# Performance work log

Measured on AMD Instinct MI355X. Metric: run time of the kernel, lower is better.

The kernel has to match this reference:

```python
import jax, jax.numpy as jnp
import numpy as np

NP, NA, D = 100000, 50000, 128


def _sage(x_src, x_dst, src, dst, Wm, bm, Wr, n_dst):
    # PyG SAGEConv: lin_l(mean_{j in N(i)} x_j) + lin_r(x_i); lin_r has no bias
    msgs = x_src[src]                                            # [E, D] gather
    summed = jax.ops.segment_sum(msgs, dst, num_segments=n_dst)  # [n_dst, D]
    cnt = jax.ops.segment_sum(jnp.ones((src.shape[0],), x_src.dtype), dst,
                              num_segments=n_dst)
    mean = summed / jnp.maximum(cnt, 1.0)[:, None]               # empty nbhd -> 0
    return mean @ Wm + bm + x_dst @ Wr


def setup_inputs() -> dict:
    key = jax.random.key(0)
    ks = jax.random.split(key, 14)
    s = 1.0 / np.sqrt(D)
    return {
        "x_paper": jax.random.normal(ks[0], (NP, D), jnp.float32),
        "x_author": jax.random.normal(ks[1], (NA, D), jnp.float32),
        "Wmsg1": jax.random.normal(ks[2], (3, D, D), jnp.float32) * s,
        "b1": jax.random.normal(ks[3], (3, D), jnp.float32) * s,
        "Wroot1": jax.random.normal(ks[4], (3, D, D), jnp.float32) * s,
        "Wmsg2": jax.random.normal(ks[5], (3, D, D), jnp.float32) * s,
        "b2": jax.random.normal(ks[6], (3, D), jnp.float32) * s,
        "Wroot2": jax.random.normal(ks[7], (3, D, D), jnp.float32) * s,
        "ei_cites_src": jax.random.randint(ks[8], (300000,), 0, NP, jnp.int64),
        "ei_cites_dst": jax.random.randint(ks[9], (300000,), 0, NP, jnp.int64),
        "ei_writes_src": jax.random.randint(ks[10], (150000,), 0, NA, jnp.int64),
        "ei_writes_dst": jax.random.randint(ks[11], (150000,), 0, NP, jnp.int64),
        "ei_wb_src": jax.random.randint(ks[12], (150000,), 0, NP, jnp.int64),
        "ei_wb_dst": jax.random.randint(ks[13], (150000,), 0, NA, jnp.int64),
    }


def reference(x_paper, x_author, Wmsg1, b1, Wroot1, Wmsg2, b2, Wroot2,
              ei_cites_src, ei_cites_dst, ei_writes_src, ei_writes_dst,
              ei_wb_src, ei_wb_dst):
    def hetero_layer(xp, xa, Wm, b, Wr):
        # HeteroConv(aggr='sum'): sum per-edge-type SAGEConv outputs per dst type
        out_p = (_sage(xp, xp, ei_cites_src, ei_cites_dst, Wm[0], b[0], Wr[0], NP)
                 + _sage(xa, xp, ei_writes_src, ei_writes_dst, Wm[1], b[1], Wr[1], NP))
        out_a = _sage(xp, xa, ei_wb_src, ei_wb_dst, Wm[2], b[2], Wr[2], NA)
        return out_p, out_a

    hp, ha = hetero_layer(x_paper, x_author, Wmsg1, b1, Wroot1)
    hp, ha = jax.nn.relu(hp), jax.nn.relu(ha)
    op, oa = hetero_layer(hp, ha, Wmsg2, b2, Wroot2)
    return op, oa
```

## Files before the change

### kernel.cpp

```cpp
#include <hip/hip_runtime.h>

typedef unsigned short u16;
typedef unsigned int u32;
typedef __bf16 bf16x8 __attribute__((ext_vector_type(8)));
typedef float f32x4 __attribute__((ext_vector_type(4)));

#define NPAPER 100000
#define NAUTH  50000
#define NROWS_ALL (2 * NPAPER + NAUTH)

struct alignas(16) U4 { u32 a, b, c, d; };
struct alignas(8)  U2 { u32 a, b; };
struct alignas(16) F4 { float x, y, z, w; };

__device__ __forceinline__ float bf2f(u16 u) {
    union { u32 i; float f; } v; v.i = ((u32)u) << 16; return v.f;
}
__device__ __forceinline__ u16 f2bf(float f) {
    union { float f; u32 i; } v; v.f = f;
    u32 u = v.i;
    return (u16)((u + 0x7FFFu + ((u >> 16) & 1u)) >> 16);
}

__device__ __forceinline__ float ldf(const void* p, size_t i, int f32) {
    return f32 ? ((const float*)p)[i] : bf2f(((const u16*)p)[i]);
}

__global__ void detect_dtypes(const int* __restrict__ e, const u32* __restrict__ x,
                              const u32* __restrict__ w, const u32* __restrict__ bb,
                              int* __restrict__ flags)
{
    int t = threadIdx.x, wave = t >> 6, lane = t & 63;
    if (wave == 0) {
        int v = e[lane];
        unsigned long long m = __ballot((lane & 1) && v == 0);
        if (lane == 0) flags[0] = (__popcll(m) >= 24) ? 1 : 0;
    } else {
        const u32* p = (wave == 1) ? x : ((wave == 2) ? w : bb);
        u32 wd = p[lane];
        int ex = (int)((wd >> 7) & 0xFFu);
        unsigned long long m = __ballot(ex >= 105 && ex <= 140);
        if (lane == 0) flags[wave] = (__popcll(m) >= 40) ? 0 : 1;
    }
}

__global__ __launch_bounds__(256) void convert_x(
    const void* __restrict__ xp, const void* __restrict__ xa,
    u16* __restrict__ xpb, u16* __restrict__ xab, const int* __restrict__ flags)
{
    int f32 = flags[1];
    size_t i = ((size_t)blockIdx.x * 256 + threadIdx.x) * 8;
    const size_t np = (size_t)NPAPER * 128, ntot = np + (size_t)NAUTH * 128;
    if (i >= ntot) return;
    const void* s; u16* d; size_t off;
    if (i < np) { s = xp; d = xpb; off = i; }
    else        { s = xa; d = xab; off = i - np; }
    alignas(16) u16 o[8];
    if (f32) {
        const F4* f = (const F4*)((const float*)s + off);
        F4 f0 = f[0], f1 = f[1];
        o[0] = f2bf(f0.x); o[1] = f2bf(f0.y); o[2] = f2bf(f0.z); o[3] = f2bf(f0.w);
        o[4] = f2bf(f1.x); o[5] = f2bf(f1.y); o[6] = f2bf(f1.z); o[7] = f2bf(f1.w);
    } else {
        *(U4*)o = *(const U4*)((const u16*)s + off);
    }
    *(U4*)(d + off) = *(const U4*)o;
}

__device__ __forceinline__ int permcol(int j) {
    int s = j >> 6, u = j & 63, c = u >> 4, fr = u & 15;
    return s * 64 + fr * 4 + c;
}

__global__ __launch_bounds__(256) void prep_weights2(
    const void* __restrict__ Wm1, const void* __restrict__ b1, const void* __restrict__ Wr1,
    const void* __restrict__ Wm2, const void* __restrict__ b2, const void* __restrict__ Wr2,
    u16* __restrict__ WTp1, u16* __restrict__ WTa1,
    float* __restrict__ biasp1, float* __restrict__ biasa1,
    u16* __restrict__ WTp2, u16* __restrict__ WTa2,
    float* __restrict__ biasp2, float* __restrict__ biasa2,
    const int* __restrict__ flags)
{
    int half = blockIdx.x >= 321;
    const void* Wm = half ? Wm2 : Wm1;
    const void* b  = half ? b2  : b1;
    const void* Wr = half ? Wr2 : Wr1;
    u16* WTp = half ? WTp2 : WTp1;
    u16* WTa = half ? WTa2 : WTa1;
    float* biasp = half ? biasp2 : biasp1;
    float* biasa = half ? biasa2 : biasa1;

    int wf = flags[2], bf = flags[3];
    int tid = (blockIdx.x - half * 321) * 256 + threadIdx.x;
    if (tid < 49152) {
        int j = tid / 384, k = tid - j * 384;
        int n = permcol(j);
        float v;
        if (k < 128)      v = ldf(Wm, k * 128 + n, wf);
        else if (k < 256) v = ldf(Wm, 16384 + (k - 128) * 128 + n, wf);
        else              v = ldf(Wr, (k - 256) * 128 + n, wf)
                            + ldf(Wr, 16384 + (k - 256) * 128 + n, wf);
        WTp[j * 384 + k] = f2bf(v);
    } else if (tid < 81920) {
        int idx = tid - 49152;
        int j = idx >> 8, k = idx & 255;
        int n = permcol(j);
        float v = (k < 128) ? ldf(Wm, 2 * 16384 + k * 128 + n, wf)
                            : ldf(Wr, 2 * 16384 + (k - 128) * 128 + n, wf);
        WTa[j * 256 + k] = f2bf(v);
    } else if (tid < 82176) {
        int i = tid - 81920;
        if (i < 128) biasp[i] = ldf(b, i, bf) + ldf(b, 128 + i, bf);
        else         biasa[i - 128] = ldf(b, 256 + (i - 128), bf);
    }
}

__global__ __launch_bounds__(256) void hist3(
    const int* __restrict__ e0d, const int* __restrict__ e1d, const int* __restrict__ e2d,
    int E0, int E1, int E2, int nb0, int nb1,
    int* __restrict__ cnt, const int* __restrict__ flags)
{
    int b = blockIdx.x;
    const int* dptr; int E, base, i;
    if (b < nb0)            { dptr = e0d; E = E0; base = 0;          i = b * 256 + threadIdx.x; }
    else if (b < nb0 + nb1) { dptr = e1d; E = E1; base = NPAPER;     i = (b - nb0) * 256 + threadIdx.x; }
    else                    { dptr = e2d; E = E2; base = 2 * NPAPER; i = (b - nb0 - nb1) * 256 + threadIdx.x; }
    if (i >= E) return;
    int d = dptr[flags[0] ? 2 * i : i];
    atomicAdd(&cnt[base + d], 1);
}

__global__ __launch_bounds__(256) void scan_blksum(
    const int* __restrict__ cnt, int N, int* __restrict__ partials)
{
    __shared__ int ws[4];
    int t = threadIdx.x, lane = t & 63, wave = t >> 6;
    int i0 = blockIdx.x * 1024 + t * 4;
    int s = 0;
    #pragma unroll
    for (int j = 0; j < 4; ++j) {
        int i = i0 + j;
        if (i < N) s += cnt[i];
    }
    #pragma unroll
    for (int off = 32; off; off >>= 1) s += __shfl_xor(s, off);
    if (lane == 0) ws[wave] = s;
    __syncthreads();
    if (t == 0) partials[blockIdx.x] = ws[0] + ws[1] + ws[2] + ws[3];
}

__global__ __launch_bounds__(256) void scan_partials(int* __restrict__ partials, int nb)
{
    __shared__ int bs[256];
    int t = threadIdx.x;
    bs[t] = (t < nb) ? partials[t] : 0;
    __syncthreads();
    for (int off = 1; off < 256; off <<= 1) {
        int u = (t >= off) ? bs[t - off] : 0;
        __syncthreads();
        bs[t] += u;
        __syncthreads();
    }
    if (t < nb) partials[t] = (t == 0) ? 0 : bs[t - 1];
}

__global__ __launch_bounds__(256) void scan_write(
    const int* __restrict__ cnt, int N, const int* __restrict__ partials,
    int* __restrict__ rowptr, int* __restrict__ cursor)
{
    __shared__ int ws[4];
    int t = threadIdx.x, lane = t & 63, wave = t >> 6;
    int i0 = blockIdx.x * 1024 + t * 4;
    int v[4];
    #pragma unroll
    for (int j = 0; j < 4; ++j) {
        int i = i0 + j;
        v[j] = (i < N) ? cnt[i] : 0;
    }
    int s = v[0] + v[1] + v[2] + v[3];
    int sc = s;
    #pragma unroll
    for (int off = 1; off < 64; off <<= 1) {
        int u = __shfl_up(sc, off);
        if (lane >= off) sc += u;
    }
    if (lane == 63) ws[wave] = sc;
    __syncthreads();
    int woff = 0;
    #pragma unroll
    for (int wv = 0; wv < 3; ++wv) if (wv < wave) woff += ws[wv];
    int run = partials[blockIdx.x] + woff + (sc - s);
    #pragma unroll
    for (int j = 0; j < 4; ++j) {
        int i = i0 + j;
        if (i < N) {
            rowptr[i] = run; cursor[i] = run;
            run += v[j];
            if (i == N - 1) rowptr[N] = run;
        }
    }
}

__global__ __launch_bounds__(256) void scatter3(
    const int* __restrict__ e0s, const int* __restrict__ e0d,
    const int* __restrict__ e1s, const int* __restrict__ e1d,
    const int* __restrict__ e2s, const int* __restrict__ e2d,
    int E0, int E1, int E2, int nb0, int nb1,
    int* __restrict__ cursor, int* __restrict__ srt,
    const int* __restrict__ flags)
{
    int b = blockIdx.x;
    const int* sptr; const int* dptr; int E, base, i;
    if (b < nb0)            { sptr = e0s; dptr = e0d; E = E0; base = 0;          i = b * 256 + threadIdx.x; }
    else if (b < nb0 + nb1) { sptr = e1s; dptr = e1d; E = E1; base = NPAPER;     i = (b - nb0) * 256 + threadIdx.x; }
    else                    { sptr = e2s; dptr = e2d; E = E2; base = 2 * NPAPER; i = (b - nb0 - nb1) * 256 + threadIdx.x; }
    if (i >= E) return;
    int ii = flags[0] ? 2 * i : i;
    int d = dptr[ii];
    int pos = atomicAdd(&cursor[base + d], 1);
    srt[pos] = sptr[ii];
}

__global__ __launch_bounds__(256) void agg_all(
    const u16* __restrict__ xp, const u16* __restrict__ xa,
    const int* __restrict__ rp_all, const int* __restrict__ srt,
    u16* __restrict__ Mp, u16* __restrict__ Ma)
{
    int r = (blockIdx.x * 256 + threadIdx.x) >> 6;
    int lane = threadIdx.x & 63;
    if (r >= NROWS_ALL) return;

    const u16* x; u32* dst;
    if (r < NPAPER)            { x = xp; dst = (u32*)(Mp + (size_t)r * 256); }
    else if (r < 2 * NPAPER)   { x = xa; dst = (u32*)(Mp + (size_t)(r - NPAPER) * 256 + 128); }
    else                       { x = xp; dst = (u32*)(Ma + (size_t)(r - 2 * NPAPER) * 128); }

    int e0 = rp_all[r], e1 = rp_all[r + 1];
    float a0 = 0.0f, a1 = 0.0f;
    for (int e = e0; e < e1; e += 4) {
        int el = e1 - 1;
        int i1 = e + 1 < e1 ? e + 1 : el;
        int i2 = e + 2 < e1 ? e + 2 : el;
        int i3 = e + 3 < e1 ? e + 3 : el;
        int s0 = srt[e], s1 = srt[i1], s2 = srt[i2], s3 = srt[i3];
        u32 p0 = ((const u32*)(x + (size_t)s0 * 128))[lane];
        u32 p1 = ((const u32*)(x + (size_t)s1 * 128))[lane];
        u32 p2 = ((const u32*)(x + (size_t)s2 * 128))[lane];
        u32 p3 = ((const u32*)(x + (size_t)s3 * 128))[lane];
        p1 = (e + 1 < e1) ? p1 : 0u;
        p2 = (e + 2 < e1) ? p2 : 0u;
        p3 = (e + 3 < e1) ? p3 : 0u;
        a0 += bf2f((u16)(p0 & 0xFFFFu)) + bf2f((u16)(p1 & 0xFFFFu))
            + bf2f((u16)(p2 & 0xFFFFu)) + bf2f((u16)(p3 & 0xFFFFu));
        a1 += bf2f((u16)(p0 >> 16)) + bf2f((u16)(p1 >> 16))
            + bf2f((u16)(p2 >> 16)) + bf2f((u16)(p3 >> 16));
    }
    float rcp = 1.0f / fmaxf((float)(e1 - e0), 1.0f);
    dst[lane] = (u32)f2bf(a0 * rcp) | ((u32)f2bf(a1 * rcp) << 16);
}

template<int K, int KM>
__device__ __forceinline__ void gemm_body(
    u16* __restrict__ Bsm, int bx,
    const u16* __restrict__ M, int Mstride, const u16* __restrict__ root,
    const u16* __restrict__ WT, const float* __restrict__ bias,
    void* __restrict__ out, int out_f32, int nrows, int relu)
{
    constexpr int KSTEPS = K / 32;
    constexpr int KSH    = KSTEPS / 2;
    constexpr int KHALF  = K / 2;
    constexpr int BLD    = KHALF + 8;
    constexpr int KC     = KHALF / 8;
    constexpr int CPT    = (128 * KC) / 256;

    int t = threadIdx.x;
    int wave = t >> 6, lane = t & 63;
    int wm = wave >> 1, wn = wave & 1;
    int fr = lane & 15, fq = lane >> 4;

    int grow0 = bx * 128;

    const u16* arow[4];
    const u16* aroot[4];
    #pragma unroll
    for (int r = 0; r < 4; ++r) {
        int row = grow0 + wm * 64 + r * 16 + fr;
        if (row >= nrows) row = nrows - 1;
        arow[r]  = M + (size_t)row * Mstride;
        aroot[r] = root + (size_t)row * 128;
    }

    f32x4 acc[4][4] = {};
    bf16x8 af[2][4];

#define LOADA(buf, gks_) do {                                              \
    int k0_ = (gks_) * 32;                                                 \
    _Pragma("unroll")                                                      \
    for (int r_ = 0; r_ < 4; ++r_) {                                       \
        const u16* p_ = (k0_ < KM) ? (arow[r_] + k0_)                      \
                                   : (aroot[r_] + (k0_ - KM));             \
        af[buf][r_] = *(const bf16x8*)(p_ + fq * 8);                       \
    }                                                                      \
} while (0)

#define STAGEB(ph_) do {                                                   \
    _Pragma("unroll")                                                      \
    for (int i_ = 0; i_ < CPT; ++i_) {                                     \
        int c_ = i_ * 256 + t;                                             \
        int col_ = c_ / KC, kc_ = c_ - col_ * KC;                          \
        U4 v_ = *(const U4*)(WT + (size_t)col_ * K + (ph_) * KHALF + kc_ * 8); \
        *(U4*)(Bsm + col_ * BLD + kc_ * 8) = v_;                           \
    }                                                                      \
} while (0)

    LOADA(0, 0);
    STAGEB(0);
    __syncthreads();

    #pragma unroll
    for (int ph = 0; ph < 2; ++ph) {
        if (ph == 1) {
            __syncthreads();
            STAGEB(1);
            __syncthreads();
        }
        #pragma unroll
        for (int ksl = 0; ksl < KSH; ++ksl) {
            int gks = ph * KSH + ksl;
            int cur = gks & 1;
            if (gks + 1 < KSTEPS) LOADA((gks + 1) & 1, gks + 1);
            bf16x8 bfv[4];
            #pragma unroll
            for (int c = 0; c < 4; ++c)
                bfv[c] = *(const bf16x8*)(Bsm + (wn * 64 + c * 16 + fr) * BLD
                                          + ksl * 32 + fq * 8);
            #pragma unroll
            for (int r = 0; r < 4; ++r)
                #pragma unroll
                for (int c = 0; c < 4; ++c)
                    acc[r][c] = __builtin_amdgcn_mfma_f32_16x16x32_bf16(
                        af[cur][r], bfv[c], acc[r][c], 0, 0, 0);
        }
    }
#undef LOADA
#undef STAGEB

    float4 b4 = *(const float4*)(bias + wn * 64 + 4 * fr);
    #pragma unroll
    for (int r = 0; r < 4; ++r) {
        #pragma unroll
        for (int g = 0; g < 4; ++g) {
            int orow = grow0 + wm * 64 + r * 16 + fq * 4 + g;
            if (orow < nrows) {
                float v0 = acc[r][0][g] + b4.x;
                float v1 = acc[r][1][g] + b4.y;
                float v2 = acc[r][2][g] + b4.z;
                float v3 = acc[r][3][g] + b4.w;
                if (relu) {
                    v0 = fmaxf(v0, 0.0f); v1 = fmaxf(v1, 0.0f);
                    v2 = fmaxf(v2, 0.0f); v3 = fmaxf(v3, 0.0f);
                }
                size_t ob = (size_t)orow * 128 + wn * 64 + 4 * fr;
                if (out_f32) {
                    float4 st = { v0, v1, v2, v3 };
                    *(float4*)((float*)out + ob) = st;
                } else {
                    U2 st;
                    st.a = (u32)f2bf(v0) | ((u32)f2bf(v1) << 16);
                    st.b = (u32)f2bf(v2) | ((u32)f2bf(v3) << 16);
                    *(U2*)((u16*)out + ob) = st;
                }
            }
        }
    }
}

__global__ __launch_bounds__(256, 3) void gemm_dual(
    const u16* __restrict__ Mp, const u16* __restrict__ fp,
    const u16* __restrict__ WTp, const float* __restrict__ bp, void* __restrict__ op,
    const u16* __restrict__ Ma, const u16* __restrict__ fa,
    const u16* __restrict__ WTa, const float* __restrict__ ba, void* __restrict__ oa,
    int out_f32, int relu, int nbp)
{
    __shared__ __align__(16) u16 Bsm[128 * 200];
    if ((int)blockIdx.x < nbp)
        gemm_body<384, 256>(Bsm, blockIdx.x, Mp, 256, fp, WTp, bp, op, out_f32, NPAPER, relu);
    else
        gemm_body<256, 128>(Bsm, blockIdx.x - nbp, Ma, 128, fa, WTa, ba, oa, out_f32, NAUTH, relu);
}

extern "C" void kernel_launch(void* const* d_in, const int* in_sizes, int n_in,
                              void* d_out, int out_size, void* d_ws, size_t ws_size,
                              hipStream_t stream)
{
    const void* xp  = d_in[0];
    const void* xa  = d_in[1];
    const void* Wm1 = d_in[2];
    const void* b1  = d_in[3];
    const void* Wr1 = d_in[4];
    const void* Wm2 = d_in[5];
    const void* b2  = d_in[6];
    const void* Wr2 = d_in[7];
    const int* e0s = (const int*)d_in[8];
    const int* e0d = (const int*)d_in[9];
    const int* e1s = (const int*)d_in[10];
    const int* e1d = (const int*)d_in[11];
    const int* e2s = (const int*)d_in[12];
    const int* e2d = (const int*)d_in[13];
    int E0 = in_sizes[8], E1 = in_sizes[10], E2 = in_sizes[12];

    char* w = (char*)d_ws;
    int*   flags  = (int*)w;
    float* biasp1 = (float*)(w + 256);
    float* biasa1 = biasp1 + 128;
    float* biasp2 = biasa1 + 128;
    float* biasa2 = biasp2 + 128;
    u16*   WTp1   = (u16*)(w + 2304);
    u16*   WTa1   = WTp1 + 49152;
    u16*   WTp2   = WTa1 + 32768;
    u16*   WTa2   = WTp2 + 49152;
    int*   rp_all = (int*)(WTa2 + 32768);
    int*   cnt_all  = rp_all + 250004;
    int*   cur_all  = cnt_all + 250000;
    int*   srt_all  = cur_all + 250000;
    u16*   xpb   = (u16*)(srt_all + 600000);
    u16*   xab   = xpb + (size_t)NPAPER * 128;
    u16*   hpw   = xab + (size_t)NAUTH * 128;
    u16*   haw   = hpw + (size_t)NPAPER * 128;
    u16*   Mp    = haw + (size_t)NAUTH * 128;
    u16*   Ma    = Mp + (size_t)NPAPER * 256;
    int*   partials = (int*)(Ma + (size_t)NAUTH * 128);

    float* outp = (float*)d_out;
    float* outa = outp + (size_t)NPAPER * 128;

    detect_dtypes<<<1, 256, 0, stream>>>(e0s, (const u32*)xp, (const u32*)Wm1,
                                         (const u32*)b1, flags);
    prep_weights2<<<642, 256, 0, stream>>>(Wm1, b1, Wr1, Wm2, b2, Wr2,
                                           WTp1, WTa1, biasp1, biasa1,
                                           WTp2, WTa2, biasp2, biasa2, flags);
    {
        size_t ntot = (size_t)(NPAPER + NAUTH) * 128;
        int nbc = (int)((ntot / 8 + 255) / 256);
        convert_x<<<nbc, 256, 0, stream>>>(xp, xa, xpb, xab, flags);
    }

    {
        hipMemsetAsync(cnt_all, 0, (size_t)NROWS_ALL * 4, stream);
        int nb0 = (E0 + 255) / 256, nb1 = (E1 + 255) / 256, nb2 = (E2 + 255) / 256;
        hist3<<<nb0 + nb1 + nb2, 256, 0, stream>>>(e0d, e1d, e2d, E0, E1, E2,
                                                   nb0, nb1, cnt_all, flags);
        int nbs = (NROWS_ALL + 1023) / 1024;
        scan_blksum<<<nbs, 256, 0, stream>>>(cnt_all, NROWS_ALL, partials);
        scan_partials<<<1, 256, 0, stream>>>(partials, nbs);
        scan_write<<<nbs, 256, 0, stream>>>(cnt_all, NROWS_ALL, partials, rp_all, cur_all);
        scatter3<<<nb0 + nb1 + nb2, 256, 0, stream>>>(e0s, e0d, e1s, e1d, e2s, e2d,
                                                      E0, E1, E2, nb0, nb1,
                                                      cur_all, srt_all, flags);
    }

    const int NBP = (NPAPER + 127) / 128;
    const int NBA = (NAUTH + 127) / 128;

    for (int layer = 0; layer < 2; ++layer) {
        const u16* fp = layer ? hpw : xpb;
        const u16* fa = layer ? haw : xab;
        void* op = layer ? (void*)outp : (void*)hpw;
        void* oa = layer ? (void*)outa : (void*)haw;
        int of32 = layer ? 1 : 0;
        const u16* WTp = layer ? WTp2 : WTp1;
        const u16* WTa = layer ? WTa2 : WTa1;
        const float* bp = layer ? biasp2 : biasp1;
        const float* ba = layer ? biasa2 : biasa1;
        int relu = layer ? 0 : 1;

        agg_all<<<(NROWS_ALL * 64 + 255) / 256, 256, 0, stream>>>(
            fp, fa, rp_all, srt_all, Mp, Ma);

        gemm_dual<<<NBP + NBA, 256, 0, stream>>>(
            Mp, fp, WTp, bp, op, Ma, fa, WTa, ba, oa, of32, relu, NBP);
    }
}
```

Measured before the change: 444.6 us.

## Use 16-byte gathers with 4 edges per wave and persistent grid-stride aggregation

The aggregation kernel now splits each wave into four 16-lane groups. Each group loads a full 256-byte bf16 row using 16-byte vector loads, so one wave processes four edges per iteration, and the partial sums are combined with cross-lane shuffles. The launch becomes a fixed 2048-block persistent grid that loops over rows and prefetches the next row's CSR bounds. The goal is fewer, wider memory transactions and lower per-row launch overhead, at the cost of shuffle reductions and lanes sitting idle when a row has few neighbours.

```diff
diff --git a/kernel.cpp b/kernel.cpp
--- a/kernel.cpp
+++ b/kernel.cpp
@@ -226,37 +226,52 @@
     const int* __restrict__ rp_all, const int* __restrict__ srt,
     u16* __restrict__ Mp, u16* __restrict__ Ma)
 {
-    int r = (blockIdx.x * 256 + threadIdx.x) >> 6;
+    int wid = (blockIdx.x * 256 + threadIdx.x) >> 6;
     int lane = threadIdx.x & 63;
+    int q = lane & 15, j = lane >> 4;
+    const int S = (gridDim.x * 256) >> 6;
+
+    int r = wid;
     if (r >= NROWS_ALL) return;
-
-    const u16* x; u32* dst;
-    if (r < NPAPER)            { x = xp; dst = (u32*)(Mp + (size_t)r * 256); }
-    else if (r < 2 * NPAPER)   { x = xa; dst = (u32*)(Mp + (size_t)(r - NPAPER) * 256 + 128); }
-    else                       { x = xp; dst = (u32*)(Ma + (size_t)(r - 2 * NPAPER) * 128); }
-
     int e0 = rp_all[r], e1 = rp_all[r + 1];
-    float a0 = 0.0f, a1 = 0.0f;
-    for (int e = e0; e < e1; e += 4) {
-        int el = e1 - 1;
-        int i1 = e + 1 < e1 ? e + 1 : el;
-        int i2 = e + 2 < e1 ? e + 2 : el;
-        int i3 = e + 3 < e1 ? e + 3 : el;
-        int s0 = srt[e], s1 = srt[i1], s2 = srt[i2], s3 = srt[i3];
-        u32 p0 = ((const u32*)(x + (size_t)s0 * 128))[lane];
-        u32 p1 = ((const u32*)(x + (size_t)s1 * 128))[lane];
-        u32 p2 = ((const u32*)(x + (size_t)s2 * 128))[lane];
-        u32 p3 = ((const u32*)(x + (size_t)s3 * 128))[lane];
-        p1 = (e + 1 < e1) ? p1 : 0u;
-        p2 = (e + 2 < e1) ? p2 : 0u;
-        p3 = (e + 3 < e1) ? p3 : 0u;
-        a0 += bf2f((u16)(p0 & 0xFFFFu)) + bf2f((u16)(p1 & 0xFFFFu))
-            + bf2f((u16)(p2 & 0xFFFFu)) + bf2f((u16)(p3 & 0xFFFFu));
-        a1 += bf2f((u16)(p0 >> 16)) + bf2f((u16)(p1 >> 16))
-            + bf2f((u16)(p2 >> 16)) + bf2f((u16)(p3 >> 16));
-    }
-    float rcp = 1.0f / fmaxf((float)(e1 - e0), 1.0f);
-    dst[lane] = (u32)f2bf(a0 * rcp) | ((u32)f2bf(a1 * rcp) << 16);
+    while (true) {
+        int rn = r + S, n0 = 0, n1 = 0;
+        if (rn < NROWS_ALL) { n0 = rp_all[rn]; n1 = rp_all[rn + 1]; }
+
+        const u16* x; u16* dst;
+        if (r < NPAPER)          { x = xp; dst = Mp + (size_t)r * 256; }
+        else if (r < 2 * NPAPER) { x = xa; dst = Mp + (size_t)(r - NPAPER) * 256 + 128; }
+        else                     { x = xp; dst = Ma + (size_t)(r - 2 * NPAPER) * 128; }
+
+        float a[8] = {};
+        for (int e = e0; e < e1; e += 4) {
+            int idx = e + j;
+            int cidx = idx < e1 ? idx : (e1 - 1);
+            int s = srt[cidx];
+            U4 pk = *(const U4*)(x + (size_t)s * 128 + q * 8);
+            if (idx >= e1) { pk.a = 0; pk.b = 0; pk.c = 0; pk.d = 0; }
+            a[0] += bf2f((u16)(pk.a & 0xFFFFu)); a[1] += bf2f((u16)(pk.a >> 16));
+            a[2] += bf2f((u16)(pk.b & 0xFFFFu)); a[3] += bf2f((u16)(pk.b >> 16));
+            a[4] += bf2f((u16)(pk.c & 0xFFFFu)); a[5] += bf2f((u16)(pk.c >> 16));
+            a[6] += bf2f((u16)(pk.d & 0xFFFFu)); a[7] += bf2f((u16)(pk.d >> 16));
+        }
+        #pragma unroll
+        for (int i = 0; i < 8; ++i) {
+            a[i] += __shfl_xor(a[i], 16);
+            a[i] += __shfl_xor(a[i], 32);
+        }
+        float rcp = 1.0f / fmaxf((float)(e1 - e0), 1.0f);
+        if (j == 0) {
+            U4 st;
+            st.a = (u32)f2bf(a[0] * rcp) | ((u32)f2bf(a[1] * rcp) << 16);
+            st.b = (u32)f2bf(a[2] * rcp) | ((u32)f2bf(a[3] * rcp) << 16);
+            st.c = (u32)f2bf(a[4] * rcp) | ((u32)f2bf(a[5] * rcp) << 16);
+            st.d = (u32)f2bf(a[6] * rcp) | ((u32)f2bf(a[7] * rcp) << 16);
+            *(U4*)(dst + q * 8) = st;
+        }
+        if (rn >= NROWS_ALL) break;
+        r = rn; e0 = n0; e1 = n1;
+    }
 }
 
 template<int K, int KM>
@@ -474,8 +489,7 @@
         const float* ba = layer ? biasa2 : biasa1;
         int relu = layer ? 0 : 1;
 
-        agg_all<<<(NROWS_ALL * 64 + 255) / 256, 256, 0, stream>>>(
-            fp, fa, rp_all, srt_all, Mp, Ma);
+        agg_all<<<2048, 256, 0, stream>>>(fp, fa, rp_all, srt_all, Mp, Ma);
 
         gemm_dual<<<NBP + NBA, 256, 0, stream>>>(
             Mp, fp, WTp, bp, op, Ma, fa, WTa, ba, oa, of32, relu, NBP);
```

Measured after the change: 450.6 us. No clear change (+1.3%).

## Fuse preprocessing kernels and process two rows per wave in aggregation

Applied to the files above, without the earlier changes.

Merges the input conversion, weight preparation and degree histogram kernels into a single launch, with block ranges dispatching to each task, and moves the count memset ahead of it. The aggregation kernel now has each wave handle two adjacent destination rows, interleaving their gather loops so more independent loads are in flight per wave. This cuts launch overhead and raises memory-level parallelism, but rows with unequal degree leave part of the wave idle and each wave uses more registers.

```diff
diff --git a/kernel.cpp b/kernel.cpp
--- a/kernel.cpp
+++ b/kernel.cpp
@@ -44,90 +44,93 @@
     }
 }
 
-__global__ __launch_bounds__(256) void convert_x(
-    const void* __restrict__ xp, const void* __restrict__ xa,
-    u16* __restrict__ xpb, u16* __restrict__ xab, const int* __restrict__ flags)
-{
-    int f32 = flags[1];
-    size_t i = ((size_t)blockIdx.x * 256 + threadIdx.x) * 8;
-    const size_t np = (size_t)NPAPER * 128, ntot = np + (size_t)NAUTH * 128;
-    if (i >= ntot) return;
-    const void* s; u16* d; size_t off;
-    if (i < np) { s = xp; d = xpb; off = i; }
-    else        { s = xa; d = xab; off = i - np; }
-    alignas(16) u16 o[8];
-    if (f32) {
-        const F4* f = (const F4*)((const float*)s + off);
-        F4 f0 = f[0], f1 = f[1];
-        o[0] = f2bf(f0.x); o[1] = f2bf(f0.y); o[2] = f2bf(f0.z); o[3] = f2bf(f0.w);
-        o[4] = f2bf(f1.x); o[5] = f2bf(f1.y); o[6] = f2bf(f1.z); o[7] = f2bf(f1.w);
-    } else {
-        *(U4*)o = *(const U4*)((const u16*)s + off);
-    }
-    *(U4*)(d + off) = *(const U4*)o;
-}
-
 __device__ __forceinline__ int permcol(int j) {
     int s = j >> 6, u = j & 63, c = u >> 4, fr = u & 15;
     return s * 64 + fr * 4 + c;
 }
 
-__global__ __launch_bounds__(256) void prep_weights2(
+__global__ __launch_bounds__(256) void fused_pre(
+    const void* __restrict__ xp, const void* __restrict__ xa,
+    u16* __restrict__ xpb, u16* __restrict__ xab,
     const void* __restrict__ Wm1, const void* __restrict__ b1, const void* __restrict__ Wr1,
     const void* __restrict__ Wm2, const void* __restrict__ b2, const void* __restrict__ Wr2,
     u16* __restrict__ WTp1, u16* __restrict__ WTa1,
     float* __restrict__ biasp1, float* __restrict__ biasa1,
     u16* __restrict__ WTp2, u16* __restrict__ WTa2,
     float* __restrict__ biasp2, float* __restrict__ biasa2,
-    const int* __restrict__ flags)
-{
-    int half = blockIdx.x >= 321;
-    const void* Wm = half ? Wm2 : Wm1;
-    const void* b  = half ? b2  : b1;
-    const void* Wr = half ? Wr2 : Wr1;
-    u16* WTp = half ? WTp2 : WTp1;
-    u16* WTa = half ? WTa2 : WTa1;
-    float* biasp = half ? biasp2 : biasp1;
-    float* biasa = half ? biasa2 : biasa1;
-
-    int wf = flags[2], bf = flags[3];
-    int tid = (blockIdx.x - half * 321) * 256 + threadIdx.x;
-    if (tid < 49152) {
-        int j = tid / 384, k = tid - j * 384;
-        int n = permcol(j);
-        float v;
-        if (k < 128)      v = ldf(Wm, k * 128 + n, wf);
-        else if (k < 256) v = ldf(Wm, 16384 + (k - 128) * 128 + n, wf);
-        else              v = ldf(Wr, (k - 256) * 128 + n, wf)
-                            + ldf(Wr, 16384 + (k - 256) * 128 + n, wf);
-        WTp[j * 384 + k] = f2bf(v);
-    } else if (tid < 81920) {
-        int idx = tid - 49152;
-        int j = idx >> 8, k = idx & 255;
-        int n = permcol(j);
-        float v = (k < 128) ? ldf(Wm, 2 * 16384 + k * 128 + n, wf)
-                            : ldf(Wr, 2 * 16384 + (k - 128) * 128 + n, wf);
-        WTa[j * 256 + k] = f2bf(v);
-    } else if (tid < 82176) {
-        int i = tid - 81920;
-        if (i < 128) biasp[i] = ldf(b, i, bf) + ldf(b, 128 + i, bf);
-        else         biasa[i - 128] = ldf(b, 256 + (i - 128), bf);
-    }
-}
-
-__global__ __launch_bounds__(256) void hist3(
     const int* __restrict__ e0d, const int* __restrict__ e1d, const int* __restrict__ e2d,
     int E0, int E1, int E2, int nb0, int nb1,
-    int* __restrict__ cnt, const int* __restrict__ flags)
+    int* __restrict__ cnt, int nbc,
+    const int* __restrict__ flags)
 {
     int b = blockIdx.x;
-    const int* dptr; int E, base, i;
-    if (b < nb0)            { dptr = e0d; E = E0; base = 0;          i = b * 256 + threadIdx.x; }
-    else if (b < nb0 + nb1) { dptr = e1d; E = E1; base = NPAPER;     i = (b - nb0) * 256 + threadIdx.x; }
-    else                    { dptr = e2d; E = E2; base = 2 * NPAPER; i = (b - nb0 - nb1) * 256 + threadIdx.x; }
-    if (i >= E) return;
-    int d = dptr[flags[0] ? 2 * i : i];
-    atomicAdd(&cnt[base + d], 1);
+    int t = threadIdx.x;
+    if (b < nbc) {
+        int f32 = flags[1];
+        size_t i = ((size_t)b * 256 + t) * 8;
+        const size_t np = (size_t)NPAPER * 128, ntot = np + (size_t)NAUTH * 128;
+        if (i >= ntot) return;
+        const void* s; u16* d; size_t off;
+        if (i < np) { s = xp; d = xpb; off = i; }
+        else        { s = xa; d = xab; off = i - np; }
+        alignas(16) u16 o[8];
+        if (f32) {
+            const F4* f = (const F4*)((const float*)s + off);
+            F4 f0 = f[0], f1 = f[1];
+            o[0] = f2bf(f0.x); o[1] = f2bf(f0.y); o[2] = f2bf(f0.z); o[3] = f2bf(f0.w);
+            o[4] = f2bf(f1.x); o[5] = f2bf(f1.y); o[6] = f2bf(f1.z); o[7] = f2bf(f1.w);
+        } else {
+            *(U4*)o = *(const U4*)((const u16*)s + off);
+        }
+        *(U4*)(d + off) = *(const U4*)o;
+        return;
+    }
+    b -= nbc;
+    if (b < 642) {
+        int half = b >= 321;
+        const void* Wm = half ? Wm2 : Wm1;
+        const void* bb = half ? b2  : b1;
+        const void* Wr = half ? Wr2 : Wr1;
+        u16* WTp = half ? WTp2 : WTp1;
+        u16* WTa = half ? WTa2 : WTa1;
+        float* biasp = half ? biasp2 : biasp1;
+        float* biasa = half ? biasa2 : biasa1;
+
+        int wf = flags[2], bf = flags[3];
+        int tid = (b - half * 321) * 256 + t;
+        if (tid < 49152) {
+            int j = tid / 384, k = tid - j * 384;
+            int n = permcol(j);
+            float v;
+            if (k < 128)      v = ldf(Wm, k * 128 + n, wf);
+            else if (k < 256) v = ldf(Wm, 16384 + (k - 128) * 128 + n, wf);
+            else              v = ldf(Wr, (k - 256) * 128 + n, wf)
+                                + ldf(Wr, 16384 + (k - 256) * 128 + n, wf);
+            WTp[j * 384 + k] = f2bf(v);
+        } else if (tid < 81920) {
+            int idx = tid - 49152;
+            int j = idx >> 8, k = idx & 255;
+            int n = permcol(j);
+            float v = (k < 128) ? ldf(Wm, 2 * 16384 + k * 128 + n, wf)
+                                : ldf(Wr, 2 * 16384 + (k - 128) * 128 + n, wf);
+            WTa[j * 256 + k] = f2bf(v);
+        } else if (tid < 82176) {
+            int i = tid - 81920;
+            if (i < 128) biasp[i] = ldf(bb, i, bf) + ldf(bb, 128 + i, bf);
+            else         biasa[i - 128] = ldf(bb, 256 + (i - 128), bf);
+        }
+        return;
+    }
+    b -= 642;
+    {
+        const int* dptr; int E, base, i;
+        if (b < nb0)            { dptr = e0d; E = E0; base = 0;          i = b * 256 + t; }
+        else if (b < nb0 + nb1) { dptr = e1d; E = E1; base = NPAPER;     i = (b - nb0) * 256 + t; }
+        else                    { dptr = e2d; E = E2; base = 2 * NPAPER; i = (b - nb0 - nb1) * 256 + t; }
+        if (i >= E) return;
+        int d = dptr[flags[0] ? 2 * i : i];
+        atomicAdd(&cnt[base + d], 1);
+    }
 }
 
 __global__ __launch_bounds__(256) void scan_blksum(
@@ -221,42 +224,70 @@
     srt[pos] = sptr[ii];
 }
 
+__device__ __forceinline__ void agg_resolve(int r, const u16* xp, const u16* xa,
+                                            u16* Mp, u16* Ma,
+                                            const u16*& x, u16*& d)
+{
+    if (r < NPAPER)          { x = xp; d = Mp + (size_t)r * 256; }
+    else if (r < 2 * NPAPER) { x = xa; d = Mp + (size_t)(r - NPAPER) * 256 + 128; }
+    else                     { x = xp; d = Ma + (size_t)(r - 2 * NPAPER) * 128; }
+}
+
 __global__ __launch_bounds__(256) void agg_all(
     const u16* __restrict__ xp, const u16* __restrict__ xa,
     const int* __restrict__ rp_all, const int* __restrict__ srt,
     u16* __restrict__ Mp, u16* __restrict__ Ma)
 {
-    int r = (blockIdx.x * 256 + threadIdx.x) >> 6;
+    int wid = (blockIdx.x * 256 + threadIdx.x) >> 6;
     int lane = threadIdx.x & 63;
-    if (r >= NROWS_ALL) return;
-
-    const u16* x; u32* dst;
-    if (r < NPAPER)            { x = xp; dst = (u32*)(Mp + (size_t)r * 256); }
-    else if (r < 2 * NPAPER)   { x = xa; dst = (u32*)(Mp + (size_t)(r - NPAPER) * 256 + 128); }
-    else                       { x = xp; dst = (u32*)(Ma + (size_t)(r - 2 * NPAPER) * 128); }
-
-    int e0 = rp_all[r], e1 = rp_all[r + 1];
-    float a0 = 0.0f, a1 = 0.0f;
-    for (int e = e0; e < e1; e += 4) {
-        int el = e1 - 1;
-        int i1 = e + 1 < e1 ? e + 1 : el;
-        int i2 = e + 2 < e1 ? e + 2 : el;
-        int i3 = e + 3 < e1 ? e + 3 : el;
-        int s0 = srt[e], s1 = srt[i1], s2 = srt[i2], s3 = srt[i3];
-        u32 p0 = ((const u32*)(x + (size_t)s0 * 128))[lane];
-        u32 p1 = ((const u32*)(x + (size_t)s1 * 128))[lane];
-        u32 p2 = ((const u32*)(x + (size_t)s2 * 128))[lane];
-        u32 p3 = ((const u32*)(x + (size_t)s3 * 128))[lane];
-        p1 = (e + 1 < e1) ? p1 : 0u;
-        p2 = (e + 2 < e1) ? p2 : 0u;
-        p3 = (e + 3 < e1) ? p3 : 0u;
-        a0 += bf2f((u16)(p0 & 0xFFFFu)) + bf2f((u16)(p1 & 0xFFFFu))
-            + bf2f((u16)(p2 & 0xFFFFu)) + bf2f((u16)(p3 & 0xFFFFu));
-        a1 += bf2f((u16)(p0 >> 16)) + bf2f((u16)(p1 >> 16))
-            + bf2f((u16)(p2 >> 16)) + bf2f((u16)(p3 >> 16));
-    }
-    float rcp = 1.0f / fmaxf((float)(e1 - e0), 1.0f);
-    dst[lane] = (u32)f2bf(a0 * rcp) | ((u32)f2bf(a1 * rcp) << 16);
+    int r0 = wid * 2;
+    if (r0 >= NROWS_ALL) return;
+    int has1 = (r0 + 1 < NROWS_ALL);
+
+    int eA0 = rp_all[r0], eA1 = rp_all[r0 + 1];
+    int eB0 = eA1, eB1 = has1 ? rp_all[r0 + 2] : eA1;
+
+    const u16 *xA, *xB; u16 *dA, *dB;
+    agg_resolve(r0, xp, xa, Mp, Ma, xA, dA);
+    agg_resolve(has1 ? r0 + 1 : r0, xp, xa, Mp, Ma, xB, dB);
+
+    float a0A = 0.0f, a1A = 0.0f, a0B = 0.0f, a1B = 0.0f;
+    int itA = (eA1 - eA0 + 3) >> 2;
+    int itB = (eB1 - eB0 + 3) >> 2;
+    int iters = itA > itB ? itA : itB;
+
+#define GATH4(e_, elast_, x_, q0_, q1_) do {                                \
+    int el_ = (elast_) - 1;                                                 \
+    int i1_ = (e_) + 1, i2_ = (e_) + 2, i3_ = (e_) + 3;                     \
+    int c1_ = i1_ < (elast_) ? i1_ : el_;                                   \
+    int c2_ = i2_ < (elast_) ? i2_ : el_;                                   \
+    int c3_ = i3_ < (elast_) ? i3_ : el_;                                   \
+    int s0_ = srt[e_], s1_ = srt[c1_], s2_ = srt[c2_], s3_ = srt[c3_];      \
+    u32 p0_ = ((const u32*)((x_) + (size_t)s0_ * 128))[lane];               \
+    u32 p1_ = ((const u32*)((x_) + (size_t)s1_ * 128))[lane];               \
+    u32 p2_ = ((const u32*)((x_) + (size_t)s2_ * 128))[lane];               \
+    u32 p3_ = ((const u32*)((x_) + (size_t)s3_ * 128))[lane];               \
+    p1_ = (i1_ < (elast_)) ? p1_ : 0u;                                      \
+    p2_ = (i2_ < (elast_)) ? p2_ : 0u;                                      \
+    p3_ = (i3_ < (elast_)) ? p3_ : 0u;                                      \
+    q0_ += bf2f((u16)(p0_ & 0xFFFFu)) + bf2f((u16)(p1_ & 0xFFFFu))          \
+         + bf2f((u16)(p2_ & 0xFFFFu)) + bf2f((u16)(p3_ & 0xFFFFu));         \
+    q1_ += bf2f((u16)(p0_ >> 16)) + bf2f((u16)(p1_ >> 16))                  \
+         + bf2f((u16)(p2_ >> 16)) + bf2f((u16)(p3_ >> 16));                 \
+} while (0)
+
+    for (int k = 0; k < iters; ++k) {
+        if (k < itA) GATH4(eA0 + 4 * k, eA1, xA, a0A, a1A);
+        if (k < itB) GATH4(eB0 + 4 * k, eB1, xB, a0B, a1B);
+    }
+#undef GATH4
+
+    float rcpA = 1.0f / fmaxf((float)(eA1 - eA0), 1.0f);
+    ((u32*)dA)[lane] = (u32)f2bf(a0A * rcpA) | ((u32)f2bf(a1A * rcpA) << 16);
+    if (has1) {
+        float rcpB = 1.0f / fmaxf((float)(eB1 - eB0), 1.0f);
+        ((u32*)dB)[lane] = (u32)f2bf(a0B * rcpB) | ((u32)f2bf(a1B * rcpB) << 16);
+    }
 }
 
 template<int K, int KM>
@@ -434,22 +465,24 @@
     float* outp = (float*)d_out;
     float* outa = outp + (size_t)NPAPER * 128;
 
+    hipMemsetAsync(cnt_all, 0, (size_t)NROWS_ALL * 4, stream);
+
     detect_dtypes<<<1, 256, 0, stream>>>(e0s, (const u32*)xp, (const u32*)Wm1,
                                          (const u32*)b1, flags);
-    prep_weights2<<<642, 256, 0, stream>>>(Wm1, b1, Wr1, Wm2, b2, Wr2,
-                                           WTp1, WTa1, biasp1, biasa1,
-                                           WTp2, WTa2, biasp2, biasa2, flags);
+
+    int nb0 = (E0 + 255) / 256, nb1 = (E1 + 255) / 256, nb2 = (E2 + 255) / 256;
+    int nbc;
     {
         size_t ntot = (size_t)(NPAPER + NAUTH) * 128;
-        int nbc = (int)((ntot / 8 + 255) / 256);
-        convert_x<<<nbc, 256, 0, stream>>>(xp, xa, xpb, xab, flags);
-    }
+        nbc = (int)((ntot / 8 + 255) / 256);
+    }
+    fused_pre<<<nbc + 642 + nb0 + nb1 + nb2, 256, 0, stream>>>(
+        xp, xa, xpb, xab,
+        Wm1, b1, Wr1, Wm2, b2, Wr2,
+        WTp1, WTa1, biasp1, biasa1, WTp2, WTa2, biasp2, biasa2,
+        e0d, e1d, e2d, E0, E1, E2, nb0, nb1, cnt_all, nbc, flags);
 
     {
-        hipMemsetAsync(cnt_all, 0, (size_t)NROWS_ALL * 4, stream);
-        int nb0 = (E0 + 255) / 256, nb1 = (E1 + 255) / 256, nb2 = (E2 + 255) / 256;
-        hist3<<<nb0 + nb1 + nb2, 256, 0, stream>>>(e0d, e1d, e2d, E0, E1, E2,
-                                                   nb0, nb1, cnt_all, flags);
         int nbs = (NROWS_ALL + 1023) / 1024;
         scan_blksum<<<nbs, 256, 0, stream>>>(cnt_all, NROWS_ALL, partials);
         scan_partials<<<1, 256, 0, stream>>>(partials, nbs);
@@ -461,6 +494,7 @@
 
     const int NBP = (NPAPER + 127) / 128;
     const int NBA = (NAUTH + 127) / 128;
+    const int NAGG = ((NROWS_ALL + 1) / 2 * 64 + 255) / 256;
 
     for (int layer = 0; layer < 2; ++layer) {
         const u16* fp = layer ? hpw : xpb;
@@ -474,8 +508,7 @@
         const float* ba = layer ? biasa2 : biasa1;
         int relu = layer ? 0 : 1;
 
-        agg_all<<<(NROWS_ALL * 64 + 255) / 256, 256, 0, stream>>>(
-            fp, fa, rp_all, srt_all, Mp, Ma);
+        agg_all<<<NAGG, 256, 0, stream>>>(fp, fa, rp_all, srt_all, Mp, Ma);
 
         gemm_dual<<<NBP + NBA, 256, 0, stream>>>(
             Mp, fp, WTp, bp, op, Ma, fa, WTa, ba, oa, of32, relu, NBP);
```

Result: faster. 419.0 us (-5.8%).
